# Optimization experiments

Measured on AMD Instinct MI355X. Metric: run time of the kernel, lower is better.

Reference implementation:

```python
import jax, jax.numpy as jnp
import numpy as np

K = 20
EPS = 1e-5  # BatchNorm eps, eval mode with running_mean=0, running_var=1


def _bn(x, g, b):
    # eval-mode BatchNorm with running stats (mean=0, var=1): affine only
    return x * (g / jnp.sqrt(1.0 + EPS)) + b


def _lrelu(x):
    return jax.nn.leaky_relu(x, 0.2)


def setup_inputs() -> dict:
    key = jax.random.key(0)
    ks = jax.random.split(key, 8)
    B, N, EMB, OUT = 8, 4096, 1024, 128
    def w(k, shape):
        fan_in = shape[0]
        return (jax.random.normal(k, shape, jnp.float32) / np.sqrt(fan_in)).astype(jnp.float32)
    inp = {
        "x":  jax.random.normal(ks[0], (B, N, 3), jnp.float32),
        "W1": w(ks[1], (6, 64)),   "g1": jnp.ones(64),  "b1": jnp.zeros(64),
        "W2": w(ks[2], (64, 64)),  "g2": jnp.ones(64),  "b2": jnp.zeros(64),
        "W3": w(ks[3], (64, 128)), "g3": jnp.ones(128), "b3": jnp.zeros(128),
        "W4": w(ks[4], (128, 256)),"g4": jnp.ones(256), "b4": jnp.zeros(256),
        "W5": w(ks[5], (512, EMB)),"g5": jnp.ones(EMB), "b5": jnp.zeros(EMB),
        "L1": w(ks[6], (2 * EMB, 512)), "g6": jnp.ones(512), "b6": jnp.zeros(512),
        "L2": w(ks[7], (512, 256)), "L2b": jnp.zeros(256), "g7": jnp.ones(256), "b7": jnp.zeros(256),
        "L3": w(jax.random.fold_in(key, 99), (256, OUT)), "L3b": jnp.zeros(OUT),
    }
    return inp


def _knn_idx(pts):
    # pts: [B, 3, N]; returns indices of K nearest neighbors [B, N, K]
    inner = -2.0 * jnp.einsum('bdn,bdm->bnm', pts, pts)  # [B,N,N]
    xx = jnp.sum(pts * pts, axis=1)                       # [B,N]
    pd = -xx[:, :, None] - inner - xx[:, None, :]          # negative squared distance
    return jax.lax.top_k(pd, K)[1]                         # [B,N,K]


def reference(x, W1, g1, b1, W2, g2, b2, W3, g3, b3, W4, g4, b4,
              W5, g5, b5, L1, g6, b6, L2, L2b, g7, b7, L3, L3b):
    B, N, _ = x.shape
    pts = jnp.transpose(x, (0, 2, 1))           # [B,3,N]
    idx = _knn_idx(pts)                          # [B,N,K]

    # gather neighbor coordinates: [B,N,K,3]
    feature = jax.vmap(lambda xb, ib: xb[ib])(x, idx)
    center = jnp.broadcast_to(x[:, :, None, :], (B, N, K, 3))
    h = jnp.concatenate([feature, center], axis=-1)  # [B,N,K,6]

    h = _lrelu(_bn(jnp.einsum('bnkc,co->bnko', h, W1), g1, b1))
    x1 = jnp.max(h, axis=2)                          # [B,N,64]
    h = _lrelu(_bn(jnp.einsum('bnkc,co->bnko', h, W2), g2, b2))
    x2 = jnp.max(h, axis=2)                          # [B,N,64]
    h = _lrelu(_bn(jnp.einsum('bnkc,co->bnko', h, W3), g3, b3))
    x3 = jnp.max(h, axis=2)                          # [B,N,128]
    h = _lrelu(_bn(jnp.einsum('bnkc,co->bnko', h, W4), g4, b4))
    x4 = jnp.max(h, axis=2)                          # [B,N,256]

    hc = jnp.concatenate([x1, x2, x3, x4], axis=-1)  # [B,N,512]
    h5 = _lrelu(_bn(jnp.einsum('bnc,co->bno', hc, W5), g5, b5))  # [B,N,EMB]

    gmax = jnp.max(h5, axis=1)                       # [B,EMB]
    gavg = jnp.mean(h5, axis=1)                      # [B,EMB]
    g = jnp.concatenate([gmax, gavg], axis=-1)       # [B,2*EMB]

    f = _lrelu(_bn(g @ L1, g6, b6))                  # dropout = identity (eval)
    f = _lrelu(_bn(f @ L2 + L2b, g7, b7))
    return f @ L3 + L3b                              # [B,OUT]
```

## Files before the change

### kernel.cpp

```cpp
#include <hip/hip_runtime.h>
#include <hip/hip_bf16.h>
#include <hip/hip_fp16.h>

#define NPTS 4096
#define KNB  20
#define EPSB 1e-5f

typedef _Float16 half8 __attribute__((ext_vector_type(8)));
typedef float    f32x4 __attribute__((ext_vector_type(4)));

__device__ __forceinline__ f32x4 mfma16(half8 a, half8 b, f32x4 c){
  return __builtin_amdgcn_mfma_f32_16x16x32_f16(a, b, c, 0, 0, 0);
}

__device__ __forceinline__ half8 loadA_lds(const _Float16* buf, int C, int mt, int ks, int lane){
  int row = mt*16 + (lane & 15);
  int k0  = ks*32 + (lane >> 4)*8;
  int e   = (row*C + k0) ^ ((row & 7) << 3);
  return *reinterpret_cast<const half8*>(&buf[e]);
}

__device__ __forceinline__ half8 loadB_g(const _Float16* WT, int K, int nt, int ks, int lane){
  int col = nt*16 + (lane & 15);
  int k0  = ks*32 + (lane >> 4)*8;
  return *reinterpret_cast<const half8*>(&WT[col*K + k0]);
}

__global__ __launch_bounds__(1024)
void knn_kernel(const float* __restrict__ x, int* __restrict__ idx_out){
  __shared__ float4 spts[NPTS];
  int b  = blockIdx.x >> 8;
  int r0 = (blockIdx.x & 255) << 4;
  const float* xb = x + (size_t)b*NPTS*3;
  for (int t = threadIdx.x; t < NPTS; t += 1024){
    float px = xb[t*3+0], py = xb[t*3+1], pz = xb[t*3+2];
    spts[t] = make_float4(px, py, pz, px*px + py*py + pz*pz);
  }
  __syncthreads();
  int wave = threadIdx.x >> 6, lane = threadIdx.x & 63;
  int i = r0 + wave;
  float4 pi = spts[i];
  float b1 = -INFINITY, b2 = -INFINITY, b3 = -INFINITY;
  int   i1 = 0, i2 = 0, i3 = 0;
  #pragma unroll 8
  for (int t = 0; t < 64; ++t){
    int j = (t << 6) + lane;
    float4 q = spts[j];
    float d = 2.f*(pi.x*q.x + pi.y*q.y + pi.z*q.z) - pi.w - q.w;
    if (d > b1){ b3=b2; i3=i2; b2=b1; i2=i1; b1=d; i1=j; }
    else if (d > b2){ b3=b2; i3=i2; b2=d; i2=j; }
    else if (d > b3){ b3=d; i3=j; }
  }
  unsigned long long rem = 0ull;
  size_t obase = ((size_t)b*NPTS + i)*KNB;
  #pragma unroll 1
  for (int kk = 0; kk < KNB; ++kk){
    float bv = b1; int bi = i1;
    #pragma unroll
    for (int m = 32; m > 0; m >>= 1){
      float ov = __shfl_xor(bv, m);
      int   oi = __shfl_xor(bi, m);
      if (ov > bv || (ov == bv && oi < bi)){ bv = ov; bi = oi; }
    }
    if (lane == 0) idx_out[obase + kk] = bi;
    if ((bi & 63) == lane){
      rem |= 1ull << (bi >> 6);
      b1 = b2; i1 = i2; b2 = b3; i2 = i3; b3 = -INFINITY; i3 = 0;
      if (b1 == -INFINITY){
        #pragma unroll 8
        for (int t = 0; t < 64; ++t){
          if (rem & (1ull << t)) continue;
          int j = (t << 6) + lane;
          float4 q = spts[j];
          float d = 2.f*(pi.x*q.x + pi.y*q.y + pi.z*q.z) - pi.w - q.w;
          if (d > b1){ b3=b2; i3=i2; b2=b1; i2=i1; b1=d; i1=j; }
          else if (d > b2){ b3=b2; i3=i2; b2=d; i2=j; }
          else if (d > b3){ b3=d; i3=j; }
        }
      }
    }
  }
}

__global__ __launch_bounds__(256)
void prep_kernel(const float* __restrict__ W2, const float* __restrict__ W3,
                 const float* __restrict__ W4, const float* __restrict__ W5,
                 _Float16* __restrict__ W2T, _Float16* __restrict__ W3T,
                 _Float16* __restrict__ W4T, _Float16* __restrict__ W5T){
  int t = blockIdx.x*256 + threadIdx.x;
  if (t < 4096){ int o=t>>6, k=t&63;                W2T[t] = (_Float16)W2[k*64+o]; }
  else if (t < 12288){ int u=t-4096;  int o=u>>6, k=u&63;   W3T[u] = (_Float16)W3[k*128+o]; }
  else if (t < 45056){ int u=t-12288; int o=u>>7, k=u&127;  W4T[u] = (_Float16)W4[k*256+o]; }
  else if (t < 569344){ int u=t-45056; int o=u>>9, k=u&511; W5T[u] = (_Float16)W5[k*1024+o]; }
}

__device__ __forceinline__ void bucket(int mt, bool c1, bool c2, bool c3, float v,
                                       float& p0, float& p1, float& p2, float& p3){
  if (mt == 0)      p0 = fmaxf(p0, v);
  else if (mt == 4) p3 = fmaxf(p3, v);
  else if (mt == 1){ p1 = fmaxf(p1, c1 ? v : -INFINITY); p0 = fmaxf(p0, c1 ? -INFINITY : v); }
  else if (mt == 2){ p2 = fmaxf(p2, c2 ? v : -INFINITY); p1 = fmaxf(p1, c2 ? -INFINITY : v); }
  else             { p3 = fmaxf(p3, c3 ? v : -INFINITY); p2 = fmaxf(p2, c3 ? -INFINITY : v); }
}

__device__ __forceinline__ void reduce_write_x(float p0, float p1, float p2, float p3,
                                               _Float16* __restrict__ hc, size_t gp0,
                                               int off, int g, int c){
  p0 = fmaxf(p0, __shfl_xor(p0, 16)); p0 = fmaxf(p0, __shfl_xor(p0, 32));
  p1 = fmaxf(p1, __shfl_xor(p1, 16)); p1 = fmaxf(p1, __shfl_xor(p1, 32));
  p2 = fmaxf(p2, __shfl_xor(p2, 16)); p2 = fmaxf(p2, __shfl_xor(p2, 32));
  p3 = fmaxf(p3, __shfl_xor(p3, 16)); p3 = fmaxf(p3, __shfl_xor(p3, 32));
  float v = (g == 0) ? p0 : (g == 1) ? p1 : (g == 2) ? p2 : p3;
  hc[(gp0 + g)*512 + off + c] = (_Float16)v;
}

__global__ __launch_bounds__(256)
void edge_kernel(const float* __restrict__ x, const int* __restrict__ knn,
                 const float* __restrict__ W1, const float* __restrict__ g1, const float* __restrict__ b1,
                 const _Float16* __restrict__ W2T, const float* __restrict__ g2, const float* __restrict__ b2,
                 const _Float16* __restrict__ W3T, const float* __restrict__ g3, const float* __restrict__ b3,
                 const _Float16* __restrict__ W4T, const float* __restrict__ g4, const float* __restrict__ b4,
                 _Float16* __restrict__ hc){
  __shared__ __align__(16) char smem[40960];
  _Float16* hb1 = (_Float16*)(smem);
  _Float16* hb2 = (_Float16*)(smem + 10240);
  _Float16* hb3 = (_Float16*)(smem + 20480);
  float*    h0f = (float*)(smem + 20480);
  float*    h0c = (float*)(smem + 20480 + 1280);
  const float rs = 1.f / sqrtf(1.f + EPSB);
  int gp0 = blockIdx.x << 2;
  int b   = gp0 >> 12;
  int n0  = gp0 & (NPTS-1);
  const float* xb = x + (size_t)b*NPTS*3;
  int tid = threadIdx.x;
  if (tid < 80){
    int p = tid / 20, k = tid % 20;
    int nb = knn[((size_t)b*NPTS + n0 + p)*KNB + k];
    h0f[tid*4+0] = xb[nb*3+0];
    h0f[tid*4+1] = xb[nb*3+1];
    h0f[tid*4+2] = xb[nb*3+2];
  } else if (tid < 96){
    int u = tid - 80; int p = u >> 2, c = u & 3;
    if (c < 3) h0c[p*4+c] = xb[(n0+p)*3+c];
  }
  __syncthreads();
  int w = tid >> 6, lane = tid & 63, g = lane >> 4, cc = lane & 15;
  bool c1 = (g >= 1), c2 = (g >= 2), c3 = (g >= 3);
  {
    int col = lane;
    float sc = g1[col]*rs, bs = b1[col];
    float w0=W1[col], w1_=W1[64+col], w2_=W1[128+col], w3_=W1[192+col], w4_=W1[256+col], w5_=W1[320+col];
    float cx = h0c[w*4+0], cy = h0c[w*4+1], cz = h0c[w*4+2];
    float m1 = -INFINITY;
    #pragma unroll 5
    for (int k = 0; k < KNB; ++k){
      int r = w*20 + k;
      float a = h0f[r*4+0]*w0 + h0f[r*4+1]*w1_ + h0f[r*4+2]*w2_ + cx*w3_ + cy*w4_ + cz*w5_;
      float vv = a*sc + bs; vv = vv > 0.f ? vv : 0.2f*vv;
      hb1[((r<<6)+col) ^ ((r&7)<<3)] = (_Float16)vv;
      m1 = fmaxf(m1, vv);
    }
    hc[(size_t)(gp0 + w)*512 + col] = (_Float16)m1;
  }
  __syncthreads();
  {
    int colg = (w<<4) + cc;
    float sc = g2[colg]*rs, bs = b2[colg];
    half8 bf0 = loadB_g(W2T, 64, w, 0, lane);
    half8 bf1 = loadB_g(W2T, 64, w, 1, lane);
    f32x4 acc[5];
    #pragma unroll
    for (int mt = 0; mt < 5; ++mt){
      f32x4 a = {0.f,0.f,0.f,0.f};
      a = mfma16(loadA_lds(hb1,64,mt,0,lane), bf0, a);
      a = mfma16(loadA_lds(hb1,64,mt,1,lane), bf1, a);
      acc[mt] = a;
    }
    float p0=-INFINITY, p1=-INFINITY, p2=-INFINITY, p3=-INFINITY;
    #pragma unroll
    for (int mt = 0; mt < 5; ++mt){
      #pragma unroll
      for (int rr = 0; rr < 4; ++rr){
        int row = mt*16 + g*4 + rr;
        float vv = acc[mt][rr]*sc + bs; vv = vv > 0.f ? vv : 0.2f*vv;
        hb2[(row*64 + colg) ^ ((row&7)<<3)] = (_Float16)vv;
        bucket(mt, c1, c2, c3, vv, p0, p1, p2, p3);
      }
    }
    reduce_write_x(p0,p1,p2,p3, hc, gp0, 64 + (w<<4), g, cc);
  }
  __syncthreads();
  #pragma unroll
  for (int tt = 0; tt < 2; ++tt){
    int nt = (w<<1) + tt;
    int colg = (nt<<4) + cc;
    float sc = g3[colg]*rs, bs = b3[colg];
    half8 bf0 = loadB_g(W3T, 64, nt, 0, lane);
    half8 bf1 = loadB_g(W3T, 64, nt, 1, lane);
    f32x4 acc[5];
    #pragma unroll
    for (int mt = 0; mt < 5; ++mt){
      f32x4 a = {0.f,0.f,0.f,0.f};
      a = mfma16(loadA_lds(hb2,64,mt,0,lane), bf0, a);
      a = mfma16(loadA_lds(hb2,64,mt,1,lane), bf1, a);
      acc[mt] = a;
    }
    float p0=-INFINITY, p1=-INFINITY, p2=-INFINITY, p3=-INFINITY;
    #pragma unroll
    for (int mt = 0; mt < 5; ++mt){
      #pragma unroll
      for (int rr = 0; rr < 4; ++rr){
        int row = mt*16 + g*4 + rr;
        float vv = acc[mt][rr]*sc + bs; vv = vv > 0.f ? vv : 0.2f*vv;
        hb3[(row*128 + colg) ^ ((row&7)<<3)] = (_Float16)vv;
        bucket(mt, c1, c2, c3, vv, p0, p1, p2, p3);
      }
    }
    reduce_write_x(p0,p1,p2,p3, hc, gp0, 128 + (nt<<4), g, cc);
  }
  __syncthreads();
  #pragma unroll 1
  for (int ch = 0; ch < 4; ++ch){
    int ntg = (ch<<2) + w;
    int colg = (ntg<<4) + cc;
    float sc = g4[colg]*rs, bs = b4[colg];
    half8 bw[4];
    #pragma unroll
    for (int ks = 0; ks < 4; ++ks) bw[ks] = loadB_g(W4T, 128, ntg, ks, lane);
    f32x4 acc[5] = {};
    #pragma unroll
    for (int ks = 0; ks < 4; ++ks)
      #pragma unroll
      for (int mt = 0; mt < 5; ++mt)
        acc[mt] = mfma16(loadA_lds(hb3,128,mt,ks,lane), bw[ks], acc[mt]);
    float p0=-INFINITY, p1=-INFINITY, p2=-INFINITY, p3=-INFINITY;
    #pragma unroll
    for (int mt = 0; mt < 5; ++mt){
      #pragma unroll
      for (int rr = 0; rr < 4; ++rr){
        float vv = acc[mt][rr]*sc + bs; vv = vv > 0.f ? vv : 0.2f*vv;
        bucket(mt, c1, c2, c3, vv, p0, p1, p2, p3);
      }
    }
    reduce_write_x(p0,p1,p2,p3, hc, gp0, 256 + (ntg<<4), g, cc);
  }
}

__global__ __launch_bounds__(256)
void gemm5_kernel(const _Float16* __restrict__ hc, const _Float16* __restrict__ W5T,
                  const float* __restrict__ g5, const float* __restrict__ b5,
                  float* __restrict__ red){
  __shared__ __align__(16) _Float16 sA[64*512];
  int rowblk = blockIdx.x >> 2;
  int colblk = blockIdx.x & 3;
  int row0 = rowblk << 6;
  #pragma unroll 1
  for (int it = 0; it < 16; ++it){
    int eoff = it*2048 + threadIdx.x*8;
    int row = eoff >> 9;
    int ine = eoff & 511;
    half8 vsrc = *reinterpret_cast<const half8*>(
        &hc[(size_t)(row0 + row)*512 + (ine ^ ((row & 7) << 3))]);
    *reinterpret_cast<half8*>(&sA[(row << 9) + ine]) = vsrc;
  }
  __syncthreads();
  int wave = threadIdx.x >> 6, lane = threadIdx.x & 63;
  f32x4 acc[4][4] = {};
  #pragma unroll 1
  for (int ks = 0; ks < 16; ++ks){
    half8 af[4];
    #pragma unroll
    for (int mt = 0; mt < 4; ++mt) af[mt] = loadA_lds(sA, 512, mt, ks, lane);
    #pragma unroll
    for (int nt = 0; nt < 4; ++nt){
      int ntg = (colblk<<4) + (wave<<2) + nt;
      half8 bf = loadB_g(W5T, 512, ntg, ks, lane);
      #pragma unroll
      for (int mt = 0; mt < 4; ++mt)
        acc[mt][nt] = mfma16(af[mt], bf, acc[mt][nt]);
    }
  }
  int batch = row0 >> 12;
  int chunk = (row0 & (NPTS-1)) >> 6;
  const float rs = 1.f/sqrtf(1.f+EPSB);
  #pragma unroll
  for (int nt = 0; nt < 4; ++nt){
    int ntg = (colblk<<4) + (wave<<2) + nt;
    int colg = (ntg<<4) + (lane & 15);
    float sc = g5[colg]*rs, bs = b5[colg];
    float vmax = -INFINITY, vsum = 0.f;
    #pragma unroll
    for (int mt = 0; mt < 4; ++mt){
      #pragma unroll
      for (int r = 0; r < 4; ++r){
        float vv = acc[mt][nt][r]*sc + bs;
        vv = vv>0.f ? vv : 0.2f*vv;
        vmax = fmaxf(vmax, vv); vsum += vv;
      }
    }
    vmax = fmaxf(vmax, __shfl_xor(vmax, 16)); vsum += __shfl_xor(vsum, 16);
    vmax = fmaxf(vmax, __shfl_xor(vmax, 32)); vsum += __shfl_xor(vsum, 32);
    if ((lane >> 4) == 0){
      size_t base = (size_t)((batch<<6) + chunk)*2048;
      red[base + colg] = vmax;
      red[base + 1024 + colg] = vsum;
    }
  }
}

__global__ __launch_bounds__(256)
void reduce_g_kernel(const float* __restrict__ red, float* __restrict__ g){
  int t = blockIdx.x*256 + threadIdx.x;
  int b = t >> 10, col = t & 1023;
  float m = -INFINITY, s = 0.f;
  #pragma unroll 4
  for (int c = 0; c < 64; ++c){
    size_t base = (size_t)((b<<6)+c)*2048;
    m = fmaxf(m, red[base + col]);
    s += red[base + 1024 + col];
  }
  g[(b<<11) + col]        = m;
  g[(b<<11) + 1024 + col] = s * (1.f/4096.f);
}

__global__ __launch_bounds__(256)
void fc1_kernel(const float* __restrict__ g, const float* __restrict__ L1,
                const float* __restrict__ g6, const float* __restrict__ b6,
                float* __restrict__ f1){
  __shared__ float part[4][64];
  int b  = blockIdx.x >> 3;
  int og = blockIdx.x & 7;
  int o  = (og << 6) + (threadIdx.x & 63);
  int kg = threadIdx.x >> 6;
  const float* gb = g + (b << 11);
  float acc = 0.f;
  #pragma unroll 8
  for (int k = kg*512; k < kg*512 + 512; ++k) acc += gb[k]*L1[k*512 + o];
  part[kg][threadIdx.x & 63] = acc;
  __syncthreads();
  if (threadIdx.x < 64){
    float s = part[0][threadIdx.x] + part[1][threadIdx.x] + part[2][threadIdx.x] + part[3][threadIdx.x];
    float v = s*(g6[o]/sqrtf(1.f+EPSB)) + b6[o];
    f1[(b<<9) + o] = v > 0.f ? v : 0.2f*v;
  }
}

__global__ __launch_bounds__(256)
void fc2_kernel(const float* __restrict__ f1, const float* __restrict__ L2, const float* __restrict__ L2b,
                const float* __restrict__ g7, const float* __restrict__ b7, float* __restrict__ f2){
  __shared__ float part[4][64];
  int b  = blockIdx.x >> 2;
  int og = blockIdx.x & 3;
  int o  = (og << 6) + (threadIdx.x & 63);
  int kg = threadIdx.x >> 6;
  const float* fb = f1 + (b << 9);
  float acc = 0.f;
  #pragma unroll 8
  for (int k = kg*128; k < kg*128 + 128; ++k) acc += fb[k]*L2[k*256 + o];
  part[kg][threadIdx.x & 63] = acc;
  __syncthreads();
  if (threadIdx.x < 64){
    float s = part[0][threadIdx.x] + part[1][threadIdx.x] + part[2][threadIdx.x] + part[3][threadIdx.x];
    float v = (s + L2b[o])*(g7[o]/sqrtf(1.f+EPSB)) + b7[o];
    f2[(b<<8) + o] = v > 0.f ? v : 0.2f*v;
  }
}

__global__ __launch_bounds__(256)
void fc3_kernel(const float* __restrict__ f2, const float* __restrict__ L3, const float* __restrict__ L3b,
                float* __restrict__ out){
  __shared__ float part[2][128];
  int b  = blockIdx.x;
  int o  = threadIdx.x & 127;
  int kg = threadIdx.x >> 7;
  const float* fb = f2 + (b << 8);
  float acc = 0.f;
  #pragma unroll 8
  for (int k = kg*128; k < kg*128 + 128; ++k) acc += fb[k]*L3[k*128 + o];
  part[kg][o] = acc;
  __syncthreads();
  if (threadIdx.x < 128)
    out[(b<<7) + o] = part[0][o] + part[1][o] + L3b[o];
}

extern "C" void kernel_launch(void* const* d_in, const int* in_sizes, int n_in,
                              void* d_out, int out_size, void* d_ws, size_t ws_size,
                              hipStream_t stream){
  const float* x  = (const float*)d_in[0];
  const float* W1 = (const float*)d_in[1];
  const float* g1 = (const float*)d_in[2];  const float* b1 = (const float*)d_in[3];
  const float* W2 = (const float*)d_in[4];
  const float* g2 = (const float*)d_in[5];  const float* b2 = (const float*)d_in[6];
  const float* W3 = (const float*)d_in[7];
  const float* g3 = (const float*)d_in[8];  const float* b3 = (const float*)d_in[9];
  const float* W4 = (const float*)d_in[10];
  const float* g4 = (const float*)d_in[11]; const float* b4 = (const float*)d_in[12];
  const float* W5 = (const float*)d_in[13];
  const float* g5 = (const float*)d_in[14]; const float* b5 = (const float*)d_in[15];
  const float* L1 = (const float*)d_in[16];
  const float* g6 = (const float*)d_in[17]; const float* b6 = (const float*)d_in[18];
  const float* L2 = (const float*)d_in[19]; const float* L2b = (const float*)d_in[20];
  const float* g7 = (const float*)d_in[21]; const float* b7 = (const float*)d_in[22];
  const float* L3 = (const float*)d_in[23]; const float* L3b = (const float*)d_in[24];

  char* ws = (char*)d_ws;
  int*      idx  = (int*)(ws + 0);
  _Float16* hc   = (_Float16*)(ws + 2621440);
  _Float16* W2T  = (_Float16*)(ws + 36175872);
  _Float16* W3T  = (_Float16*)(ws + 36184064);
  _Float16* W4T  = (_Float16*)(ws + 36200448);
  _Float16* W5T  = (_Float16*)(ws + 36265984);
  float*    red  = (float*)(ws + 37314560);
  float*    gbuf = (float*)(ws + 41508864);
  float*    f1   = (float*)(ws + 41574400);
  float*    f2   = (float*)(ws + 41590784);

  knn_kernel<<<2048, 1024, 0, stream>>>(x, idx);
  prep_kernel<<<2224, 256, 0, stream>>>(W2, W3, W4, W5, W2T, W3T, W4T, W5T);
  edge_kernel<<<8192, 256, 0, stream>>>(x, idx, W1, g1, b1, W2T, g2, b2,
                                        W3T, g3, b3, W4T, g4, b4, hc);
  gemm5_kernel<<<2048, 256, 0, stream>>>(hc, W5T, g5, b5, red);
  reduce_g_kernel<<<32, 256, 0, stream>>>(red, gbuf);
  fc1_kernel<<<64, 256, 0, stream>>>(gbuf, L1, g6, b6, f1);
  fc2_kernel<<<32, 256, 0, stream>>>(f1, L2, L2b, g7, b7, f2);
  fc3_kernel<<<8, 256, 0, stream>>>(f2, L3, L3b, (float*)d_out);
}
```

Measured before the change: 470.8 us.

## Pack KNN distance/index into sortable u64 keys and use half-wave per query

The KNN kernel now processes two query points per wave, each handled by 32 lanes, so each block covers 32 rows and the grid is halved, which also halves the redundant point loads into LDS. Distances and indices are packed into a single order-preserving 64-bit key, so the top-3 insertion and the 5-step butterfly reduction compare one value instead of a value plus a tiebreak index. The refill rescan no longer uses a removed-bitmask; it skips any key at or above the last selected one. Each lane now scans 128 candidates instead of 64, and the 64-bit compares and shuffles may cost more per step.

Measured after the change: 567.2 us. 20.5% more time.

```diff
diff --git a/kernel.cpp b/kernel.cpp
--- a/kernel.cpp
+++ b/kernel.cpp
@@ -8,6 +8,7 @@
 
 typedef _Float16 half8 __attribute__((ext_vector_type(8)));
 typedef float    f32x4 __attribute__((ext_vector_type(4)));
+typedef unsigned long long u64;
 
 __device__ __forceinline__ f32x4 mfma16(half8 a, half8 b, f32x4 c){
   return __builtin_amdgcn_mfma_f32_16x16x32_f16(a, b, c, 0, 0, 0);
@@ -29,8 +30,8 @@
 __global__ __launch_bounds__(1024)
 void knn_kernel(const float* __restrict__ x, int* __restrict__ idx_out){
   __shared__ float4 spts[NPTS];
-  int b  = blockIdx.x >> 8;
-  int r0 = (blockIdx.x & 255) << 4;
+  int b  = blockIdx.x >> 7;
+  int r0 = (blockIdx.x & 127) << 5;
   const float* xb = x + (size_t)b*NPTS*3;
   for (int t = threadIdx.x; t < NPTS; t += 1024){
     float px = xb[t*3+0], py = xb[t*3+1], pz = xb[t*3+2];
@@ -38,44 +39,50 @@
   }
   __syncthreads();
   int wave = threadIdx.x >> 6, lane = threadIdx.x & 63;
-  int i = r0 + wave;
+  int half = lane >> 5, l31 = lane & 31;
+  int i = r0 + wave*2 + half;
   float4 pi = spts[i];
-  float b1 = -INFINITY, b2 = -INFINITY, b3 = -INFINITY;
-  int   i1 = 0, i2 = 0, i3 = 0;
+  u64 k1 = 0, k2 = 0, k3 = 0;
   #pragma unroll 8
-  for (int t = 0; t < 64; ++t){
-    int j = (t << 6) + lane;
+  for (int t = 0; t < 128; ++t){
+    int j = (t << 5) + l31;
     float4 q = spts[j];
     float d = 2.f*(pi.x*q.x + pi.y*q.y + pi.z*q.z) - pi.w - q.w;
-    if (d > b1){ b3=b2; i3=i2; b2=b1; i2=i1; b1=d; i1=j; }
-    else if (d > b2){ b3=b2; i3=i2; b2=d; i2=j; }
-    else if (d > b3){ b3=d; i3=j; }
-  }
-  unsigned long long rem = 0ull;
+    unsigned s = __float_as_uint(d);
+    unsigned key = s ^ ((unsigned)(((int)s) >> 31) | 0x80000000u);
+    u64 k = ((u64)key << 32) | (unsigned)(~j);
+    if (k > k1){ k3 = k2; k2 = k1; k1 = k; }
+    else if (k > k2){ k3 = k2; k2 = k; }
+    else if (k > k3){ k3 = k; }
+  }
   size_t obase = ((size_t)b*NPTS + i)*KNB;
   #pragma unroll 1
   for (int kk = 0; kk < KNB; ++kk){
-    float bv = b1; int bi = i1;
-    #pragma unroll
-    for (int m = 32; m > 0; m >>= 1){
-      float ov = __shfl_xor(bv, m);
-      int   oi = __shfl_xor(bi, m);
-      if (ov > bv || (ov == bv && oi < bi)){ bv = ov; bi = oi; }
-    }
-    if (lane == 0) idx_out[obase + kk] = bi;
-    if ((bi & 63) == lane){
-      rem |= 1ull << (bi >> 6);
-      b1 = b2; i1 = i2; b2 = b3; i2 = i3; b3 = -INFINITY; i3 = 0;
-      if (b1 == -INFINITY){
+    u64 bv = k1;
+    #pragma unroll
+    for (int m = 1; m <= 16; m <<= 1){
+      u64 ov = __shfl_xor(bv, m);
+      if (ov > bv) bv = ov;
+    }
+    if (l31 == 0) idx_out[obase + kk] = (int)~(unsigned)bv;
+    bool won = (k1 == bv);
+    k1 = won ? k2 : k1;
+    k2 = won ? k3 : k2;
+    k3 = won ? 0ull : k3;
+    if (kk < KNB-1 && __any(k1 == 0ull)){
+      if (k1 == 0ull){
         #pragma unroll 8
-        for (int t = 0; t < 64; ++t){
-          if (rem & (1ull << t)) continue;
-          int j = (t << 6) + lane;
+        for (int t = 0; t < 128; ++t){
+          int j = (t << 5) + l31;
           float4 q = spts[j];
           float d = 2.f*(pi.x*q.x + pi.y*q.y + pi.z*q.z) - pi.w - q.w;
-          if (d > b1){ b3=b2; i3=i2; b2=b1; i2=i1; b1=d; i1=j; }
-          else if (d > b2){ b3=b2; i3=i2; b2=d; i2=j; }
-          else if (d > b3){ b3=d; i3=j; }
+          unsigned s = __float_as_uint(d);
+          unsigned key = s ^ ((unsigned)(((int)s) >> 31) | 0x80000000u);
+          u64 k = ((u64)key << 32) | (unsigned)(~j);
+          if (k >= bv) continue;
+          if (k > k1){ k3 = k2; k2 = k1; k1 = k; }
+          else if (k > k2){ k3 = k2; k2 = k; }
+          else if (k > k3){ k3 = k; }
         }
       }
     }
@@ -415,7 +422,7 @@
   float*    f1   = (float*)(ws + 41574400);
   float*    f2   = (float*)(ws + 41590784);
 
-  knn_kernel<<<2048, 1024, 0, stream>>>(x, idx);
+  knn_kernel<<<1024, 1024, 0, stream>>>(x, idx);
   prep_kernel<<<2224, 256, 0, stream>>>(W2, W3, W4, W5, W2T, W3T, W4T, W5T);
   edge_kernel<<<8192, 256, 0, stream>>>(x, idx, W1, g1, b1, W2T, g2, b2,
                                         W3T, g3, b3, W4T, g4, b4, hc);
```
